# Kernel optimization log

Hardware: AMD Instinct MI355X
Metric: run time of the kernel (lower is better)

The kernel has to match this reference:

```python
import jax, jax.numpy as jnp
import numpy as np

EPS = 1e-06


def _feature_map(x):
    # elu(x) + 1  (elu with alpha=1)
    return jnp.where(x > 0, x + 1.0, jnp.exp(x))


def setup_inputs() -> dict:
    key = jax.random.key(0)
    k1, k2, k3 = jax.random.split(key, 3)
    N, L, S, H, D = 4, 8192, 8192, 8, 64
    q = jax.random.normal(k1, (N, L, H, D), dtype=jnp.float32)
    k = jax.random.normal(k2, (N, S, H, D), dtype=jnp.float32)
    v = jax.random.normal(k3, (N, S, H, D), dtype=jnp.float32)
    q_mask = jnp.ones((N, L), dtype=jnp.float32)
    kv_mask = jnp.ones((N, S), dtype=jnp.float32)
    return {"q": q, "k": k, "v": v, "q_mask": q_mask, "kv_mask": kv_mask}


def reference(q, k, v, q_mask, kv_mask):
    # Linear attention with elu+1 feature map (Katharopoulos et al.)
    qf = _feature_map(q)  # [N, L, H, D]
    kf = _feature_map(k)  # [N, S, H, D]
    qf = q_mask[:, :, None, None] * qf
    kf = kv_mask[:, :, None, None] * kf
    vm = kv_mask[:, :, None, None] * v
    S = v.shape[1]
    # global KV state: [N, H, D, Dv]; v scaled by 1/S for numerical stability
    kv = jnp.einsum('nshd,nshv->nhdv', kf, vm / S)
    # normalizer: einsum('nlhd,nshd->nlh') == q . sum_s(k)
    k_sum = kf.sum(axis=1)  # [N, H, D]
    div = 1.0 / (jnp.einsum('nlhd,nhd->nlh', qf, k_sum) + EPS)
    out = S * jnp.einsum('nlhd,nhdv,nlh->nlhv', qf, kv, div)
    return out
```

## Files before the change

### kernel.cpp

```cpp
#include <hip/hip_runtime.h>
#include <math.h>


#define EPS 1e-6f

static constexpr int Nc = 4;
static constexpr int Lc = 8192;
static constexpr int Sc = 8192;
static constexpr int Hc = 8;
static constexpr int NH = Nc * Hc;
static constexpr int STATE = 64 * 64 + 64;
static constexpr int TS = 32;
static constexpr int TSP = 36;
static constexpr int QSP = 68;

typedef __attribute__((ext_vector_type(4))) short short4v;
typedef __attribute__((ext_vector_type(8))) short short8v;
typedef __attribute__((ext_vector_type(4))) float f32x4;

__device__ __forceinline__ float fmap(float x) {
    return x > 0.f ? x + 1.f : __expf(x);
}
__device__ __forceinline__ unsigned short f2bf(float x) {
    unsigned int u = __float_as_uint(x);
    u += 0x7FFFu + ((u >> 16) & 1u);
    return (unsigned short)(u >> 16);
}
__device__ __forceinline__ float bf2f(unsigned short h) {
    return __uint_as_float(((unsigned int)h) << 16);
}
__device__ __forceinline__ short8v ld8(const unsigned short* p) {
    short4v a = *(const short4v*)p;
    short4v b = *(const short4v*)(p + 4);
    return __builtin_shufflevector(a, b, 0, 1, 2, 3, 4, 5, 6, 7);
}
__device__ __forceinline__ unsigned int pack2(unsigned short a, unsigned short b) {
    return (unsigned)a | ((unsigned)b << 16);
}

__global__ __launch_bounds__(256, 4) void k1_partial(
    const float* __restrict__ kg, const float* __restrict__ vg,
    const float* __restrict__ kv_mask,
    float* __restrict__ partial, int chunks, int sc)
{
    __shared__ unsigned short kTh[64][TSP], kTl[64][TSP];
    __shared__ unsigned short vTh[64][TSP], vTl[64][TSP];
    __shared__ float ksb[16][64];

    const int bid = blockIdx.x;
    const int pair = bid / chunks;
    const int chunk = bid - pair * chunks;
    const int n = pair >> 3;
    const int h = pair & 7;
    const int s0 = chunk * sc;
    const int t = threadIdx.x;
    const int g = t >> 4;
    const int c4 = (t & 15) * 4;
    const int lane = t & 63;
    const int wv = t >> 6;
    const int row16 = lane & 15;
    const int g8 = (lane >> 4) * 8;

    f32x4 acc[4] = {{0.f,0.f,0.f,0.f},{0.f,0.f,0.f,0.f},
                    {0.f,0.f,0.f,0.f},{0.f,0.f,0.f,0.f}};
    float ksm[4] = {0.f, 0.f, 0.f, 0.f};

    const size_t rowstride = (size_t)Hc * 64;
    const size_t gbase = ((size_t)n * Sc * Hc + h) * 64 + c4;
    const int mbase = n * Sc;

    auto issue = [&](int sbase, float4& a0, float4& a1, float4& b0, float4& b1,
                     float& me, float& mo) {
        const int s = s0 + sbase + 2 * g;
        const size_t be = gbase + (size_t)s * rowstride;
        a0 = *(const float4*)(kg + be);
        a1 = *(const float4*)(kg + be + rowstride);
        b0 = *(const float4*)(vg + be);
        b1 = *(const float4*)(vg + be + rowstride);
        me = kv_mask[mbase + s];
        mo = kv_mask[mbase + s + 1];
    };

    auto process = [&](const float4& ck0, const float4& ck1,
                       const float4& cv0, const float4& cv1,
                       float cme, float cmo) {
        const float* kep = &ck0.x;
        const float* kop = &ck1.x;
        const float* vep = &cv0.x;
        const float* vop = &cv1.x;
        #pragma unroll
        for (int j = 0; j < 4; ++j) {
            const float fe = cme * fmap(kep[j]);
            const float fo = cmo * fmap(kop[j]);
            ksm[j] += fe + fo;
            const unsigned short he = f2bf(fe), ho = f2bf(fo);
            const unsigned short le = f2bf(fe - bf2f(he)), lo_ = f2bf(fo - bf2f(ho));
            *(unsigned int*)&kTh[c4 + j][2 * g] = pack2(he, ho);
            *(unsigned int*)&kTl[c4 + j][2 * g] = pack2(le, lo_);
            const float ue = cme * vep[j];
            const float uo = cmo * vop[j];
            const unsigned short vhe = f2bf(ue), vho = f2bf(uo);
            const unsigned short vle = f2bf(ue - bf2f(vhe)), vlo = f2bf(uo - bf2f(vho));
            *(unsigned int*)&vTh[c4 + j][2 * g] = pack2(vhe, vho);
            *(unsigned int*)&vTl[c4 + j][2 * g] = pack2(vle, vlo);
        }
        __syncthreads();

        const short8v Ah = ld8(&kTh[wv * 16 + row16][g8]);
        const short8v Al = ld8(&kTl[wv * 16 + row16][g8]);
        #pragma unroll
        for (int bt = 0; bt < 4; ++bt) {
            const short8v Bh = ld8(&vTh[bt * 16 + row16][g8]);
            const short8v Bl = ld8(&vTl[bt * 16 + row16][g8]);
            acc[bt] = __builtin_amdgcn_mfma_f32_16x16x32_bf16(Ah, Bh, acc[bt], 0, 0, 0);
            acc[bt] = __builtin_amdgcn_mfma_f32_16x16x32_bf16(Al, Bh, acc[bt], 0, 0, 0);
            acc[bt] = __builtin_amdgcn_mfma_f32_16x16x32_bf16(Ah, Bl, acc[bt], 0, 0, 0);
        }
        __syncthreads();
    };

    float4 ka0, ka1, va0, va1, kb0, kb1, vb0, vb1;
    float mea, moa, meb, mob;

    issue(0, ka0, ka1, va0, va1, mea, moa);
    for (int sb = 0; sb < sc; sb += 2 * TS) {
        issue(sb + TS, kb0, kb1, vb0, vb1, meb, mob);
        process(ka0, ka1, va0, va1, mea, moa);
        const int na = (sb + 2 * TS < sc) ? sb + 2 * TS : sb;
        issue(na, ka0, ka1, va0, va1, mea, moa);
        process(kb0, kb1, vb0, vb1, meb, mob);
    }

    float* outp = partial + (size_t)bid * STATE;
    float (*outs)[QSP] = reinterpret_cast<float (*)[QSP]>(&kTh[0][0]);
    #pragma unroll
    for (int bt = 0; bt < 4; ++bt) {
        #pragma unroll
        for (int r = 0; r < 4; ++r) {
            const int row = wv * 16 + (lane >> 4) * 4 + r;
            outs[row][bt * 16 + row16] = acc[bt][r];
        }
    }
    __syncthreads();
    #pragma unroll
    for (int p = 0; p < 4; ++p) {
        const int f = t + p * 256;
        const int row = f >> 4;
        const int cc = (f & 15) * 4;
        *(float4*)(outp + row * 64 + cc) = *(const float4*)&outs[row][cc];
    }

    *(f32x4*)&ksb[g][c4] = (f32x4){ksm[0], ksm[1], ksm[2], ksm[3]};
    __syncthreads();
    if (t < 64) {
        float s = 0.f;
        #pragma unroll
        for (int i = 0; i < 16; ++i) s += ksb[i][t];
        outp[4096 + t] = s;
    }
}

__global__ __launch_bounds__(256) void k2_reduce(
    const float* __restrict__ src, float* __restrict__ dst, int nred)
{
    const int p = blockIdx.x / 5;
    const int seg = blockIdx.x - p * 5;
    const int e4 = seg * 256 + threadIdx.x;
    if (e4 >= STATE / 4) return;
    const float4* s = (const float4*)(src + (size_t)p * nred * STATE) + e4;
    float4 acc = make_float4(0.f, 0.f, 0.f, 0.f);
    #pragma unroll 4
    for (int j = 0; j < nred; ++j) {
        float4 x = s[(size_t)j * (STATE / 4)];
        acc.x += x.x; acc.y += x.y; acc.z += x.z; acc.w += x.w;
    }
    ((float4*)(dst + (size_t)p * STATE))[e4] = acc;
}

__global__ __launch_bounds__(256) void k2b_finalize(
    const float* __restrict__ src, float* __restrict__ dst, int nred)
{
    __shared__ float kv[64][QSP];
    __shared__ float kss[64];

    const int pair = blockIdx.x;
    const int t = threadIdx.x;
    const float4* sbase = (const float4*)(src + (size_t)pair * nred * STATE);

    #pragma unroll
    for (int i = 0; i < 4; ++i) {
        const int e4 = t + i * 256;
        float4 a = make_float4(0.f, 0.f, 0.f, 0.f);
        for (int j = 0; j < nred; ++j) {
            float4 x = sbase[(size_t)j * (STATE / 4) + e4];
            a.x += x.x; a.y += x.y; a.z += x.z; a.w += x.w;
        }
        *(float4*)&kv[e4 >> 4][(e4 & 15) * 4] = a;
    }
    if (t < 16) {
        float4 a = make_float4(0.f, 0.f, 0.f, 0.f);
        for (int j = 0; j < nred; ++j) {
            float4 x = sbase[(size_t)j * (STATE / 4) + 1024 + t];
            a.x += x.x; a.y += x.y; a.z += x.z; a.w += x.w;
        }
        *(float4*)&kss[t * 4] = a;
    }
    __syncthreads();

    unsigned int* dw = (unsigned int*)(dst + (size_t)pair * STATE);
    #pragma unroll
    for (int i = 0; i < 8; ++i) {
        const int w = t + i * 256;
        const int dv = w >> 5;
        const int d0 = (w & 31) * 2;
        const float f0 = kv[d0][dv];
        const float f1 = kv[d0 + 1][dv];
        const unsigned short h0 = f2bf(f0), h1 = f2bf(f1);
        dw[w] = pack2(h0, h1);
        dw[2048 + w] = pack2(f2bf(f0 - bf2f(h0)), f2bf(f1 - bf2f(h1)));
    }
    if (t < 64) dst[(size_t)pair * STATE + 4096 + t] = kss[t];
}

__global__ __launch_bounds__(256, 4) void k3_out(
    const float* __restrict__ qg, const float* __restrict__ state,
    const float* __restrict__ q_mask, float* __restrict__ outg)
{
    __shared__ __align__(16) unsigned short qsp[2][64][QSP];
    __shared__ unsigned short kvt[2][64][QSP];
    __shared__ float ksum[64];
    __shared__ float dinv[64];

    const int nblk = Lc / 64;
    const int bid = blockIdx.x;
    const int pair = bid / nblk;
    const int lblk = bid - pair * nblk;
    const int n = pair >> 3;
    const int h = pair & 7;
    const int l0 = lblk * 64;
    const int t = threadIdx.x;
    const int lane = t & 63;
    const int wv = t >> 6;
    const int row16 = lane & 15;
    const int g8 = (lane >> 4) * 8;

    const unsigned int* sw = (const unsigned int*)(state + (size_t)pair * STATE);
    #pragma unroll
    for (int i = 0; i < 8; ++i) {
        const int w = t + i * 256;
        const int dv = w >> 5;
        const int d2 = (w & 31) * 2;
        *(unsigned int*)&kvt[0][dv][d2] = sw[w];
        *(unsigned int*)&kvt[1][dv][d2] = sw[2048 + w];
    }
    if (t < 64) ksum[t] = ((const float*)state)[(size_t)pair * STATE + 4096 + t];
    __syncthreads();

    #pragma unroll
    for (int p = 0; p < 4; ++p) {
        const int f = t + p * 256;
        const int row = f >> 4;
        const int c4 = (f & 15) * 4;
        const int l = l0 + row;
        const size_t base = ((size_t)(n * Lc + l) * Hc + h) * 64 + c4;
        const float4 qq = *(const float4*)(qg + base);
        const float m = q_mask[n * Lc + l];
        const float q0 = m * fmap(qq.x), q1 = m * fmap(qq.y);
        const float q2 = m * fmap(qq.z), q3 = m * fmap(qq.w);
        const unsigned short h0 = f2bf(q0), h1 = f2bf(q1), h2 = f2bf(q2), h3 = f2bf(q3);
        *(unsigned int*)&qsp[0][row][c4]     = pack2(h0, h1);
        *(unsigned int*)&qsp[0][row][c4 + 2] = pack2(h2, h3);
        *(unsigned int*)&qsp[1][row][c4]     = pack2(f2bf(q0 - bf2f(h0)), f2bf(q1 - bf2f(h1)));
        *(unsigned int*)&qsp[1][row][c4 + 2] = pack2(f2bf(q2 - bf2f(h2)), f2bf(q3 - bf2f(h3)));
        float dp = q0 * ksum[c4] + q1 * ksum[c4 + 1] + q2 * ksum[c4 + 2] + q3 * ksum[c4 + 3];
        dp += __shfl_xor(dp, 1);
        dp += __shfl_xor(dp, 2);
        dp += __shfl_xor(dp, 4);
        dp += __shfl_xor(dp, 8);
        if ((t & 15) == 0) dinv[row] = 1.0f / (dp + EPS);
    }
    __syncthreads();

    f32x4 acc[4] = {{0.f,0.f,0.f,0.f},{0.f,0.f,0.f,0.f},
                    {0.f,0.f,0.f,0.f},{0.f,0.f,0.f,0.f}};
    #pragma unroll
    for (int ks = 0; ks < 2; ++ks) {
        const short8v Ah = ld8(&qsp[0][wv * 16 + row16][ks * 32 + g8]);
        const short8v Al = ld8(&qsp[1][wv * 16 + row16][ks * 32 + g8]);
        #pragma unroll
        for (int bt = 0; bt < 4; ++bt) {
            const short8v Bh = ld8(&kvt[0][bt * 16 + row16][ks * 32 + g8]);
            const short8v Bl = ld8(&kvt[1][bt * 16 + row16][ks * 32 + g8]);
            acc[bt] = __builtin_amdgcn_mfma_f32_16x16x32_bf16(Ah, Bh, acc[bt], 0, 0, 0);
            acc[bt] = __builtin_amdgcn_mfma_f32_16x16x32_bf16(Al, Bh, acc[bt], 0, 0, 0);
            acc[bt] = __builtin_amdgcn_mfma_f32_16x16x32_bf16(Ah, Bl, acc[bt], 0, 0, 0);
        }
    }
    __syncthreads();

    float (*outs)[QSP] = reinterpret_cast<float (*)[QSP]>(&qsp[0][0][0]);
    #pragma unroll
    for (int bt = 0; bt < 4; ++bt) {
        #pragma unroll
        for (int r = 0; r < 4; ++r) {
            const int row = wv * 16 + (lane >> 4) * 4 + r;
            outs[row][bt * 16 + row16] = acc[bt][r] * dinv[row];
        }
    }
    __syncthreads();

    #pragma unroll
    for (int p = 0; p < 4; ++p) {
        const int f = t + p * 256;
        const int row = f >> 4;
        const int c4 = (f & 15) * 4;
        const size_t base = ((size_t)(n * Lc + l0 + row) * Hc + h) * 64 + c4;
        *(float4*)(outg + base) = *(const float4*)&outs[row][c4];
    }
}

extern "C" void kernel_launch(void* const* d_in, const int* in_sizes, int n_in,
                              void* d_out, int out_size, void* d_ws, size_t ws_size,
                              hipStream_t stream)
{
    (void)in_sizes; (void)n_in; (void)out_size;
    const float* q       = (const float*)d_in[0];
    const float* k       = (const float*)d_in[1];
    const float* v       = (const float*)d_in[2];
    const float* q_mask  = (const float*)d_in[3];
    const float* kv_mask = (const float*)d_in[4];
    float* out = (float*)d_out;

    const size_t stBytes  = (size_t)STATE * sizeof(float);
    const size_t finBytes = (size_t)NH * stBytes;
    const size_t p2Bytes  = (size_t)NH * 4 * stBytes;

    float* fin = (float*)d_ws;
    float* p2  = (float*)((char*)d_ws + finBytes);
    float* p1  = (float*)((char*)d_ws + finBytes + p2Bytes);

    int chunks = 0;
    for (int c = 32; c >= 8; c >>= 1) {
        if (ws_size >= finBytes + p2Bytes + (size_t)NH * c * stBytes) { chunks = c; break; }
    }

    if (chunks >= 8) {
        k1_partial<<<NH * chunks, 256, 0, stream>>>(k, v, kv_mask, p1, chunks, Sc / chunks);
        k2_reduce<<<NH * 4 * 5, 256, 0, stream>>>(p1, p2, chunks / 4);
        k2b_finalize<<<NH, 256, 0, stream>>>(p2, fin, 4);
    } else {
        float* p1fb = (float*)((char*)d_ws + finBytes);
        k1_partial<<<NH, 256, 0, stream>>>(k, v, kv_mask, p1fb, 1, Sc);
        k2b_finalize<<<NH, 256, 0, stream>>>(p1fb, fin, 1);
    }

    k3_out<<<NH * (Lc / 64), 256, 0, stream>>>(q, fin, q_mask, out);
}
```

Before: 79.16 us.

## Fuse partial reduction with finalize and process two L tiles per output block

Merges the two-stage reduction of per-chunk KV partials and the bf16 hi/lo finalize into a single kernel that reduces directly into the split-precision layout, dropping one launch and an intermediate buffer. The output kernel now handles two consecutive 64-row tiles per block, halving the grid and amortizing the per-block load of the KV state into shared memory. The fused reduction uses fewer blocks with longer serial loops, and the output kernel serializes its two tiles, which may reduce latency hiding.

New measurement: 74.70 us. 5.6% less time.

```diff
diff --git a/kernel.cpp b/kernel.cpp
--- a/kernel.cpp
+++ b/kernel.cpp
@@ -160,66 +160,42 @@
     }
 }
 
-__global__ __launch_bounds__(256) void k2_reduce(
+__global__ __launch_bounds__(256) void k2c_reduce_finalize(
     const float* __restrict__ src, float* __restrict__ dst, int nred)
 {
-    const int p = blockIdx.x / 5;
-    const int seg = blockIdx.x - p * 5;
-    const int e4 = seg * 256 + threadIdx.x;
-    if (e4 >= STATE / 4) return;
-    const float4* s = (const float4*)(src + (size_t)p * nred * STATE) + e4;
-    float4 acc = make_float4(0.f, 0.f, 0.f, 0.f);
+    const int b = blockIdx.x;
+    const int pair = b >> 1;
+    const int sub = b & 1;
+    const int t = threadIdx.x;
+    const int ep = sub * 256 + t;
+    const int d0 = (ep >> 4) * 2;
+    const int c4 = (ep & 15) * 4;
+
+    const float* sbase = src + (size_t)pair * nred * STATE;
+    f32x4 a0 = {0.f,0.f,0.f,0.f}, a1 = {0.f,0.f,0.f,0.f};
     #pragma unroll 4
     for (int j = 0; j < nred; ++j) {
-        float4 x = s[(size_t)j * (STATE / 4)];
-        acc.x += x.x; acc.y += x.y; acc.z += x.z; acc.w += x.w;
-    }
-    ((float4*)(dst + (size_t)p * STATE))[e4] = acc;
-}
-
-__global__ __launch_bounds__(256) void k2b_finalize(
-    const float* __restrict__ src, float* __restrict__ dst, int nred)
-{
-    __shared__ float kv[64][QSP];
-    __shared__ float kss[64];
-
-    const int pair = blockIdx.x;
-    const int t = threadIdx.x;
-    const float4* sbase = (const float4*)(src + (size_t)pair * nred * STATE);
-
+        const float* pj = sbase + (size_t)j * STATE;
+        a0 += *(const f32x4*)(pj + (size_t)d0 * 64 + c4);
+        a1 += *(const f32x4*)(pj + (size_t)(d0 + 1) * 64 + c4);
+    }
+
+    unsigned int* dw = (unsigned int*)(dst + (size_t)pair * STATE);
     #pragma unroll
     for (int i = 0; i < 4; ++i) {
-        const int e4 = t + i * 256;
-        float4 a = make_float4(0.f, 0.f, 0.f, 0.f);
-        for (int j = 0; j < nred; ++j) {
-            float4 x = sbase[(size_t)j * (STATE / 4) + e4];
-            a.x += x.x; a.y += x.y; a.z += x.z; a.w += x.w;
-        }
-        *(float4*)&kv[e4 >> 4][(e4 & 15) * 4] = a;
-    }
-    if (t < 16) {
-        float4 a = make_float4(0.f, 0.f, 0.f, 0.f);
-        for (int j = 0; j < nred; ++j) {
-            float4 x = sbase[(size_t)j * (STATE / 4) + 1024 + t];
-            a.x += x.x; a.y += x.y; a.z += x.z; a.w += x.w;
-        }
-        *(float4*)&kss[t * 4] = a;
-    }
-    __syncthreads();
-
-    unsigned int* dw = (unsigned int*)(dst + (size_t)pair * STATE);
-    #pragma unroll
-    for (int i = 0; i < 8; ++i) {
-        const int w = t + i * 256;
-        const int dv = w >> 5;
-        const int d0 = (w & 31) * 2;
-        const float f0 = kv[d0][dv];
-        const float f1 = kv[d0 + 1][dv];
-        const unsigned short h0 = f2bf(f0), h1 = f2bf(f1);
+        const int w = (c4 + i) * 32 + (d0 >> 1);
+        const unsigned short h0 = f2bf(a0[i]), h1 = f2bf(a1[i]);
         dw[w] = pack2(h0, h1);
-        dw[2048 + w] = pack2(f2bf(f0 - bf2f(h0)), f2bf(f1 - bf2f(h1)));
-    }
-    if (t < 64) dst[(size_t)pair * STATE + 4096 + t] = kss[t];
+        dw[2048 + w] = pack2(f2bf(a0[i] - bf2f(h0)), f2bf(a1[i] - bf2f(h1)));
+    }
+
+    if (sub == 0 && t < 16) {
+        f32x4 a = {0.f,0.f,0.f,0.f};
+        #pragma unroll 4
+        for (int j = 0; j < nred; ++j)
+            a += *(const f32x4*)(sbase + (size_t)j * STATE + 4096 + t * 4);
+        *(f32x4*)(dst + (size_t)pair * STATE + 4096 + t * 4) = a;
+    }
 }
 
 __global__ __launch_bounds__(256, 4) void k3_out(
@@ -231,13 +207,12 @@
     __shared__ float ksum[64];
     __shared__ float dinv[64];
 
-    const int nblk = Lc / 64;
+    const int nblk = 64;
     const int bid = blockIdx.x;
     const int pair = bid / nblk;
-    const int lblk = bid - pair * nblk;
+    const int lb = (bid - pair * nblk) * 2;
     const int n = pair >> 3;
     const int h = pair & 7;
-    const int l0 = lblk * 64;
     const int t = threadIdx.x;
     const int lane = t & 63;
     const int wv = t >> 6;
@@ -256,66 +231,71 @@
     if (t < 64) ksum[t] = ((const float*)state)[(size_t)pair * STATE + 4096 + t];
     __syncthreads();
 
-    #pragma unroll
-    for (int p = 0; p < 4; ++p) {
-        const int f = t + p * 256;
-        const int row = f >> 4;
-        const int c4 = (f & 15) * 4;
-        const int l = l0 + row;
-        const size_t base = ((size_t)(n * Lc + l) * Hc + h) * 64 + c4;
-        const float4 qq = *(const float4*)(qg + base);
-        const float m = q_mask[n * Lc + l];
-        const float q0 = m * fmap(qq.x), q1 = m * fmap(qq.y);
-        const float q2 = m * fmap(qq.z), q3 = m * fmap(qq.w);
-        const unsigned short h0 = f2bf(q0), h1 = f2bf(q1), h2 = f2bf(q2), h3 = f2bf(q3);
-        *(unsigned int*)&qsp[0][row][c4]     = pack2(h0, h1);
-        *(unsigned int*)&qsp[0][row][c4 + 2] = pack2(h2, h3);
-        *(unsigned int*)&qsp[1][row][c4]     = pack2(f2bf(q0 - bf2f(h0)), f2bf(q1 - bf2f(h1)));
-        *(unsigned int*)&qsp[1][row][c4 + 2] = pack2(f2bf(q2 - bf2f(h2)), f2bf(q3 - bf2f(h3)));
-        float dp = q0 * ksum[c4] + q1 * ksum[c4 + 1] + q2 * ksum[c4 + 2] + q3 * ksum[c4 + 3];
-        dp += __shfl_xor(dp, 1);
-        dp += __shfl_xor(dp, 2);
-        dp += __shfl_xor(dp, 4);
-        dp += __shfl_xor(dp, 8);
-        if ((t & 15) == 0) dinv[row] = 1.0f / (dp + EPS);
-    }
-    __syncthreads();
-
-    f32x4 acc[4] = {{0.f,0.f,0.f,0.f},{0.f,0.f,0.f,0.f},
-                    {0.f,0.f,0.f,0.f},{0.f,0.f,0.f,0.f}};
-    #pragma unroll
-    for (int ks = 0; ks < 2; ++ks) {
-        const short8v Ah = ld8(&qsp[0][wv * 16 + row16][ks * 32 + g8]);
-        const short8v Al = ld8(&qsp[1][wv * 16 + row16][ks * 32 + g8]);
+    for (int tl = 0; tl < 2; ++tl) {
+        const int l0 = (lb + tl) * 64;
+
+        #pragma unroll
+        for (int p = 0; p < 4; ++p) {
+            const int f = t + p * 256;
+            const int row = f >> 4;
+            const int c4 = (f & 15) * 4;
+            const int l = l0 + row;
+            const size_t base = ((size_t)(n * Lc + l) * Hc + h) * 64 + c4;
+            const float4 qq = *(const float4*)(qg + base);
+            const float m = q_mask[n * Lc + l];
+            const float q0 = m * fmap(qq.x), q1 = m * fmap(qq.y);
+            const float q2 = m * fmap(qq.z), q3 = m * fmap(qq.w);
+            const unsigned short h0 = f2bf(q0), h1 = f2bf(q1), h2 = f2bf(q2), h3 = f2bf(q3);
+            *(unsigned int*)&qsp[0][row][c4]     = pack2(h0, h1);
+            *(unsigned int*)&qsp[0][row][c4 + 2] = pack2(h2, h3);
+            *(unsigned int*)&qsp[1][row][c4]     = pack2(f2bf(q0 - bf2f(h0)), f2bf(q1 - bf2f(h1)));
+            *(unsigned int*)&qsp[1][row][c4 + 2] = pack2(f2bf(q2 - bf2f(h2)), f2bf(q3 - bf2f(h3)));
+            float dp = q0 * ksum[c4] + q1 * ksum[c4 + 1] + q2 * ksum[c4 + 2] + q3 * ksum[c4 + 3];
+            dp += __shfl_xor(dp, 1);
+            dp += __shfl_xor(dp, 2);
+            dp += __shfl_xor(dp, 4);
+            dp += __shfl_xor(dp, 8);
+            if ((t & 15) == 0) dinv[row] = 1.0f / (dp + EPS);
+        }
+        __syncthreads();
+
+        f32x4 acc[4] = {{0.f,0.f,0.f,0.f},{0.f,0.f,0.f,0.f},
+                        {0.f,0.f,0.f,0.f},{0.f,0.f,0.f,0.f}};
+        #pragma unroll
+        for (int ks = 0; ks < 2; ++ks) {
+            const short8v Ah = ld8(&qsp[0][wv * 16 + row16][ks * 32 + g8]);
+            const short8v Al = ld8(&qsp[1][wv * 16 + row16][ks * 32 + g8]);
+            #pragma unroll
+            for (int bt = 0; bt < 4; ++bt) {
+                const short8v Bh = ld8(&kvt[0][bt * 16 + row16][ks * 32 + g8]);
+                const short8v Bl = ld8(&kvt[1][bt * 16 + row16][ks * 32 + g8]);
+                acc[bt] = __builtin_amdgcn_mfma_f32_16x16x32_bf16(Ah, Bh, acc[bt], 0, 0, 0);
+                acc[bt] = __builtin_amdgcn_mfma_f32_16x16x32_bf16(Al, Bh, acc[bt], 0, 0, 0);
+                acc[bt] = __builtin_amdgcn_mfma_f32_16x16x32_bf16(Ah, Bl, acc[bt], 0, 0, 0);
+            }
+        }
+        __syncthreads();
+
+        float (*outs)[QSP] = reinterpret_cast<float (*)[QSP]>(&qsp[0][0][0]);
         #pragma unroll
         for (int bt = 0; bt < 4; ++bt) {
-            const short8v Bh = ld8(&kvt[0][bt * 16 + row16][ks * 32 + g8]);
-            const short8v Bl = ld8(&kvt[1][bt * 16 + row16][ks * 32 + g8]);
-            acc[bt] = __builtin_amdgcn_mfma_f32_16x16x32_bf16(Ah, Bh, acc[bt], 0, 0, 0);
-            acc[bt] = __builtin_amdgcn_mfma_f32_16x16x32_bf16(Al, Bh, acc[bt], 0, 0, 0);
-            acc[bt] = __builtin_amdgcn_mfma_f32_16x16x32_bf16(Ah, Bl, acc[bt], 0, 0, 0);
-        }
-    }
-    __syncthreads();
-
-    float (*outs)[QSP] = reinterpret_cast<float (*)[QSP]>(&qsp[0][0][0]);
-    #pragma unroll
-    for (int bt = 0; bt < 4; ++bt) {
-        #pragma unroll
-        for (int r = 0; r < 4; ++r) {
-            const int row = wv * 16 + (lane >> 4) * 4 + r;
-            outs[row][bt * 16 + row16] = acc[bt][r] * dinv[row];
-        }
-    }
-    __syncthreads();
-
-    #pragma unroll
-    for (int p = 0; p < 4; ++p) {
-        const int f = t + p * 256;
-        const int row = f >> 4;
-        const int c4 = (f & 15) * 4;
-        const size_t base = ((size_t)(n * Lc + l0 + row) * Hc + h) * 64 + c4;
-        *(float4*)(outg + base) = *(const float4*)&outs[row][c4];
+            #pragma unroll
+            for (int r = 0; r < 4; ++r) {
+                const int row = wv * 16 + (lane >> 4) * 4 + r;
+                outs[row][bt * 16 + row16] = acc[bt][r] * dinv[row];
+            }
+        }
+        __syncthreads();
+
+        #pragma unroll
+        for (int p = 0; p < 4; ++p) {
+            const int f = t + p * 256;
+            const int row = f >> 4;
+            const int c4 = (f & 15) * 4;
+            const size_t base = ((size_t)(n * Lc + l0 + row) * Hc + h) * 64 + c4;
+            *(float4*)(outg + base) = *(const float4*)&outs[row][c4];
+        }
+        __syncthreads();
     }
 }
 
@@ -333,26 +313,22 @@
 
     const size_t stBytes  = (size_t)STATE * sizeof(float);
     const size_t finBytes = (size_t)NH * stBytes;
-    const size_t p2Bytes  = (size_t)NH * 4 * stBytes;
 
     float* fin = (float*)d_ws;
-    float* p2  = (float*)((char*)d_ws + finBytes);
-    float* p1  = (float*)((char*)d_ws + finBytes + p2Bytes);
+    float* p1  = (float*)((char*)d_ws + finBytes);
 
     int chunks = 0;
     for (int c = 32; c >= 8; c >>= 1) {
-        if (ws_size >= finBytes + p2Bytes + (size_t)NH * c * stBytes) { chunks = c; break; }
+        if (ws_size >= finBytes + (size_t)NH * c * stBytes) { chunks = c; break; }
     }
 
     if (chunks >= 8) {
         k1_partial<<<NH * chunks, 256, 0, stream>>>(k, v, kv_mask, p1, chunks, Sc / chunks);
-        k2_reduce<<<NH * 4 * 5, 256, 0, stream>>>(p1, p2, chunks / 4);
-        k2b_finalize<<<NH, 256, 0, stream>>>(p2, fin, 4);
+        k2c_reduce_finalize<<<NH * 2, 256, 0, stream>>>(p1, fin, chunks);
     } else {
-        float* p1fb = (float*)((char*)d_ws + finBytes);
-        k1_partial<<<NH, 256, 0, stream>>>(k, v, kv_mask, p1fb, 1, Sc);
-        k2b_finalize<<<NH, 256, 0, stream>>>(p1fb, fin, 1);
-    }
-
-    k3_out<<<NH * (Lc / 64), 256, 0, stream>>>(q, fin, q_mask, out);
-}
+        k1_partial<<<NH, 256, 0, stream>>>(k, v, kv_mask, p1, 1, Sc);
+        k2c_reduce_finalize<<<NH * 2, 256, 0, stream>>>(p1, fin, 1);
+    }
+
+    k3_out<<<NH * 64, 256, 0, stream>>>(q, fin, q_mask, out);
+}
```
